# Optimization experiments

Measured on AMD Instinct MI355X. Metric: run time of the kernel, lower is better.

The kernel has to match this reference:

```python
import jax, jax.numpy as jnp
import numpy as np

D_HEAD = 64
EPS_NORM = 1e-6
EPS_COS = 1e-6


def rms_norm(x, scale, eps=EPS_NORM):
    mean_sq = jnp.mean(x * x, axis=-1, keepdims=True)
    return x * (scale * jax.lax.rsqrt(mean_sq + eps))


def setup_inputs() -> dict:
    key = jax.random.key(0)
    ks = jax.random.split(key, 8)
    b, l, d, d_ff = 2, 2048, 1024, 3072
    std = 1.0 / np.sqrt(d)
    return {
        "x": jax.random.normal(ks[0], (b, l, d), jnp.float32),
        "pos": jax.random.normal(ks[1], (b, l, 2), jnp.float32),
        "norm_scale": jnp.ones((d,), jnp.float32),
        "w_qkv": jax.random.normal(ks[2], (3 * d, d), jnp.float32) * std,
        "attn_scale": jnp.full((d // D_HEAD,), 10.0, jnp.float32),
        "w_out": jax.random.normal(ks[3], (d, d), jnp.float32) * std,
        "ff_norm_scale": jnp.ones((d,), jnp.float32),
        "w_up": jax.random.normal(ks[4], (2 * d_ff, d), jnp.float32) * std,
        "w_down": jax.random.normal(ks[5], (d, d_ff), jnp.float32) * (1.0 / np.sqrt(d_ff)),
    }


def reference(x, pos, norm_scale, w_qkv, attn_scale, w_out, ff_norm_scale, w_up, w_down):
    n, l, d = x.shape
    nh = d // D_HEAD

    # ---- self-attention block ----
    skip = x
    xn = rms_norm(x, norm_scale)
    qkv = xn @ w_qkv.T                                    # [n, l, 3d]
    qkv = qkv.reshape(n, l, 3, nh, D_HEAD).transpose(2, 0, 3, 1, 4)  # [3, n, nh, l, e]
    q, k, v = qkv[0], qkv[1], qkv[2]

    # cosine-similarity rescaling with per-head learned scale
    s = attn_scale[:, None, None]                         # [nh, 1, 1]
    sqrt_s = jnp.sqrt(s)
    q = q * (sqrt_s * jax.lax.rsqrt(jnp.sum(q * q, axis=-1, keepdims=True) + EPS_COS))
    k = k * (sqrt_s * jax.lax.rsqrt(jnp.sum(k * k, axis=-1, keepdims=True) + EPS_COS))

    # SDPA with scale=1.0 (no RoPE: rope_cls=None)
    scores = jnp.einsum("nhqe,nhke->nhqk", q, k)
    attn = jax.nn.softmax(scores, axis=-1)
    o = jnp.einsum("nhqk,nhke->nhqe", attn, v)            # [n, nh, l, e]
    o = o.transpose(0, 2, 1, 3).reshape(n, l, d)
    x = o @ w_out.T + skip

    # ---- feed-forward block (SwiGLU) ----
    skip = x
    xn = rms_norm(x, ff_norm_scale)
    u = xn @ w_up.T                                       # [n, l, 2*d_ff]
    a, g = jnp.split(u, 2, axis=-1)
    h = a * jax.nn.silu(g)
    x = h @ w_down.T + skip
    return x
```

## Files before the change

kernel.cpp:

```cpp
#include <hip/hip_runtime.h>
#include <cstdint>
#include <cstddef>
#include <cstdio>


typedef unsigned short u16;
typedef __bf16 bf16x8 __attribute__((ext_vector_type(8)));
typedef short  s16x4  __attribute__((ext_vector_type(4)));
typedef short  s16x8  __attribute__((ext_vector_type(8)));
typedef float  f32x4  __attribute__((ext_vector_type(4)));

__device__ __forceinline__ u16 f2b(float f) {
  return __builtin_bit_cast(u16, (__bf16)f);
}
__device__ __forceinline__ float b2f(u16 u) {
  return (float)__builtin_bit_cast(__bf16, u);
}

__device__ __forceinline__ void cp16(const u16* g, u16* l) {
  __builtin_amdgcn_global_load_lds(
      (__attribute__((address_space(1))) void*)(uintptr_t)g,
      (__attribute__((address_space(3))) void*)(uintptr_t)l,
      16, 0, 0);
}

template <int MODE, int BN>
__global__ __launch_bounds__(256) void gemm_bt(
    const u16* __restrict__ A, const u16* __restrict__ B,
    float* __restrict__ Cf, u16* __restrict__ Cb, const float* __restrict__ res,
    int M, int N, int K, int lda)
{
  constexpr int NI = BN / 32;
  __shared__ __align__(16) u16 lsA[128 * 64];
  __shared__ __align__(16) u16 lsB[BN * 64];
  const int t = threadIdx.x;
  const int w = t >> 6, lane = t & 63;
  const int wm = (w >> 1) * 64, wn = (w & 1) * (BN / 2);
  const int lr = lane & 15, quad = lane >> 4;
  const int cswz = lr & 7;
  const size_t rowA0 = (size_t)blockIdx.x * 128;
  const size_t rowB0 = (size_t)blockIdx.y * BN;
  const int kpb = K / (int)gridDim.z;
  const int kz0 = (int)blockIdx.z * kpb;

  f32x4 acc[4][NI] = {};

  for (int k0 = kz0; k0 < kz0 + kpb; k0 += 64) {
#pragma unroll
    for (int i = 0; i < 4; ++i) {
      const int id = i * 256 + t;
      const int r = id >> 3;
      const int c = ((id & 7) ^ (r & 7)) * 8;
      cp16(A + (rowA0 + r) * lda + k0 + c, lsA + id * 8);
    }
#pragma unroll
    for (int i = 0; i < BN / 32; ++i) {
      const int id = i * 256 + t;
      const int r = id >> 3;
      const int c = ((id & 7) ^ (r & 7)) * 8;
      cp16(B + (rowB0 + r) * (size_t)K + k0 + c, lsB + id * 8);
    }
    __syncthreads();
#pragma unroll
    for (int ks = 0; ks < 2; ++ks) {
      const int co = ((ks * 4 + quad) ^ cswz) * 8;
      bf16x8 af[4], bfr[NI];
#pragma unroll
      for (int i = 0; i < 4; ++i)
        af[i] = *(const bf16x8*)(lsA + (wm + i * 16 + lr) * 64 + co);
#pragma unroll
      for (int i = 0; i < NI; ++i)
        bfr[i] = *(const bf16x8*)(lsB + (wn + i * 16 + lr) * 64 + co);
#pragma unroll
      for (int mi = 0; mi < 4; ++mi)
#pragma unroll
        for (int ni = 0; ni < NI; ++ni)
          acc[mi][ni] = __builtin_amdgcn_mfma_f32_16x16x32_bf16(
              af[mi], bfr[ni], acc[mi][ni], 0, 0, 0);
    }
    __syncthreads();
  }

#pragma unroll
  for (int mi = 0; mi < 4; ++mi) {
#pragma unroll
    for (int r = 0; r < 4; ++r) {
      const size_t m = rowA0 + wm + mi * 16 + quad * 4 + r;
#pragma unroll
      for (int ni = 0; ni < NI; ++ni) {
        const size_t n = rowB0 + wn + ni * 16 + lr;
        const size_t o = m * (size_t)N + n;
        const float v = acc[mi][ni][r];
        if (MODE == 0) Cf[o] = v;
        else if (MODE == 1) Cf[o] = v + res[o];
        else if (MODE == 2) Cb[o] = f2b(v);
        else atomicAdd(&Cf[o], v);
      }
    }
  }
}

__global__ __launch_bounds__(256) void rmsnorm_k(
    const float* __restrict__ x, const float* __restrict__ g, u16* __restrict__ out)
{
  const int row = blockIdx.x;
  const int t = threadIdx.x;
  const float4 a = ((const float4*)(x + (size_t)row * 1024))[t];
  float ss = a.x * a.x + a.y * a.y + a.z * a.z + a.w * a.w;
#pragma unroll
  for (int o = 32; o; o >>= 1) ss += __shfl_xor(ss, o, 64);
  __shared__ float red[4];
  if ((t & 63) == 0) red[t >> 6] = ss;
  __syncthreads();
  ss = red[0] + red[1] + red[2] + red[3];
  const float r = rsqrtf(ss * (1.0f / 1024.0f) + 1e-6f);
  const float4 gg = ((const float4*)g)[t];
  ushort4 o4;
  o4.x = f2b(a.x * gg.x * r);
  o4.y = f2b(a.y * gg.y * r);
  o4.z = f2b(a.z * gg.z * r);
  o4.w = f2b(a.w * gg.w * r);
  ((ushort4*)out)[(size_t)row * 256 + t] = o4;
}

__global__ __launch_bounds__(256) void cvt_bf16_k(
    const float* __restrict__ in, u16* __restrict__ out)
{
  const size_t i = (size_t)blockIdx.x * 256 + threadIdx.x;
  const float4 v = ((const float4*)in)[i];
  ushort4 o4;
  o4.x = f2b(v.x); o4.y = f2b(v.y); o4.z = f2b(v.z); o4.w = f2b(v.w);
  ((ushort4*)out)[i] = o4;
}

__global__ __launch_bounds__(256) void qkv_prep_k(
    const u16* __restrict__ qkv, const float* __restrict__ attn_scale,
    u16* __restrict__ Qb, u16* __restrict__ Kb, u16* __restrict__ Vt)
{
  const int l0 = blockIdx.x * 64;
  const int h  = blockIdx.y;
  const int nb = blockIdx.z;
  const int t = threadIdx.x, w = t >> 6, lane = t & 63;
  __shared__ float lsV[64][65];
  const float sq = sqrtf(attn_scale[h]);
  const int head = nb * 16 + h;
#pragma unroll 4
  for (int i = 0; i < 16; ++i) {
    const int lrow = i * 4 + w;
    const int l = l0 + lrow;
    const u16* base = qkv + ((size_t)nb * 2048 + l) * 3072 + h * 64 + lane;
    const float qv = b2f(base[0]);
    const float kv = b2f(base[1024]);
    const float vv = b2f(base[2048]);
    float ssq = qv * qv, ssk = kv * kv;
#pragma unroll
    for (int o = 32; o; o >>= 1) {
      ssq += __shfl_xor(ssq, o, 64);
      ssk += __shfl_xor(ssk, o, 64);
    }
    const size_t gb = ((size_t)head * 2048 + l) * 64 + lane;
    Qb[gb] = f2b(qv * sq * rsqrtf(ssq + 1e-6f));
    Kb[gb] = f2b(kv * sq * rsqrtf(ssk + 1e-6f));
    lsV[lrow][lane] = vv;
  }
  __syncthreads();
  const int e = t >> 2, p = t & 3;
  union { u16 s[16]; uint4 v[2]; } tmp;
#pragma unroll
  for (int cc = 0; cc < 2; ++cc) {
    const int c = 2 * p + cc;
    const int kb = 32 * (c >> 2) + 4 * (c & 3);
#pragma unroll
    for (int i = 0; i < 4; ++i) {
      tmp.s[cc * 8 + i]     = f2b(lsV[kb + i][e]);
      tmp.s[cc * 8 + 4 + i] = f2b(lsV[kb + 16 + i][e]);
    }
  }
  u16* dst = Vt + ((size_t)head * 64 + e) * 2048 + l0 + p * 16;
  *(uint4*)dst = tmp.v[0];
  *(uint4*)(dst + 8) = tmp.v[1];
}

__global__ __launch_bounds__(256) void attn_k(
    const u16* __restrict__ Qb, const u16* __restrict__ Kb,
    const u16* __restrict__ Vt, u16* __restrict__ O)
{
  const int l0 = blockIdx.x * 64;
  const int head = blockIdx.y;
  const int nb = head >> 4, h = head & 15;
  const int t = threadIdx.x, w = t >> 6, lane = t & 63;
  const int lr = lane & 15, quad = lane >> 4;
  const int kh = w & 1, qh = w >> 1;
  __shared__ __align__(16) u16 lsKV[2][2][64 * 64];
  const size_t hb = (size_t)head << 17;

  const int sr = t >> 3;
  const int sc = ((t & 7) ^ (sr & 7)) * 8;
  const u16* Kg = Kb + hb + (size_t)sr * 64 + sc;
  const u16* Vg = Vt + hb + (size_t)sr * 2048 + sc;

  bf16x8 qf[2][2];
#pragma unroll
  for (int qb = 0; qb < 2; ++qb) {
    const u16* qp = Qb + hb + (size_t)(l0 + qh * 32 + qb * 16 + lr) * 64 + quad * 8;
    qf[qb][0] = *(const bf16x8*)qp;
    qf[qb][1] = *(const bf16x8*)(qp + 32);
  }

  f32x4 ot[2][4] = {};
  float rs[2] = {0.f, 0.f};

  cp16(Kg, lsKV[0][0] + t * 8);
  cp16(Kg + 32 * 64, lsKV[0][0] + 32 * 64 + t * 8);
  cp16(Vg, lsKV[0][1] + t * 8);
  cp16(Vg + 32 * 2048, lsKV[0][1] + 32 * 64 + t * 8);

  int cur = 0;
  for (int k0 = 0; k0 < 2048; k0 += 64) {
    __syncthreads();
    if (k0 + 64 < 2048) {
      const int nxt = cur ^ 1;
      const u16* Kn = Kg + (size_t)(k0 + 64) * 64;
      const u16* Vn = Vg + (k0 + 64);
      cp16(Kn, lsKV[nxt][0] + t * 8);
      cp16(Kn + 32 * 64, lsKV[nxt][0] + 32 * 64 + t * 8);
      cp16(Vn, lsKV[nxt][1] + t * 8);
      cp16(Vn + 32 * 2048, lsKV[nxt][1] + 32 * 64 + t * 8);
    }
    const u16* kb = lsKV[cur][0];
    const u16* vb = lsKV[cur][1];

    s16x4 pf[2][2];
#pragma unroll
    for (int ktl = 0; ktl < 2; ++ktl) {
      const int kt = kh * 2 + ktl;
      const int krow = (kt * 16 + lr) * 64;
      const int kswz = lr & 7;
      const bf16x8 a0 = *(const bf16x8*)(kb + krow + ((quad ^ kswz) << 3));
      const bf16x8 a1 = *(const bf16x8*)(kb + krow + (((4 + quad) ^ kswz) << 3));
#pragma unroll
      for (int qb = 0; qb < 2; ++qb) {
        f32x4 s = {};
        s = __builtin_amdgcn_mfma_f32_16x16x32_bf16(a0, qf[qb][0], s, 0, 0, 0);
        s = __builtin_amdgcn_mfma_f32_16x16x32_bf16(a1, qf[qb][1], s, 0, 0, 0);
#pragma unroll
        for (int r = 0; r < 4; ++r) {
          const float p = __expf(s[r]);
          rs[qb] += p;
          pf[qb][ktl][r] = (short)f2b(p);
        }
      }
    }
#pragma unroll
    for (int ei = 0; ei < 4; ++ei) {
      const int vrow = ei * 16 + lr;
      const s16x8 vv = *(const s16x8*)(vb + vrow * 64 + (((kh * 4 + quad) ^ (vrow & 7)) << 3));
      const s16x4 v0 = __builtin_shufflevector(vv, vv, 0, 1, 2, 3);
      const s16x4 v1 = __builtin_shufflevector(vv, vv, 4, 5, 6, 7);
#pragma unroll
      for (int qb = 0; qb < 2; ++qb) {
        ot[qb][ei] = __builtin_amdgcn_mfma_f32_16x16x16bf16_1k(v0, pf[qb][0], ot[qb][ei], 0, 0, 0);
        ot[qb][ei] = __builtin_amdgcn_mfma_f32_16x16x16bf16_1k(v1, pf[qb][1], ot[qb][ei], 0, 0, 0);
      }
    }
    cur ^= 1;
  }

#pragma unroll
  for (int qb = 0; qb < 2; ++qb) {
    rs[qb] += __shfl_xor(rs[qb], 16, 64);
    rs[qb] += __shfl_xor(rs[qb], 32, 64);
  }

  __syncthreads();
  float* mb = (float*)lsKV;
  if (kh == 1) {
    float* dst = mb + (qh * 64 + lane) * 34;
#pragma unroll
    for (int qb = 0; qb < 2; ++qb)
#pragma unroll
      for (int ei = 0; ei < 4; ++ei)
#pragma unroll
        for (int r = 0; r < 4; ++r)
          dst[qb * 16 + ei * 4 + r] = ot[qb][ei][r];
    dst[32] = rs[0];
    dst[33] = rs[1];
  }
  __syncthreads();
  if (kh == 0) {
    const float* src = mb + (qh * 64 + lane) * 34;
#pragma unroll
    for (int qb = 0; qb < 2; ++qb) {
      const float inv = 1.0f / (rs[qb] + src[32 + qb]);
      u16* ob = O + ((size_t)nb * 2048 + l0 + qh * 32 + qb * 16 + lr) * 1024 + h * 64 + quad * 4;
#pragma unroll
      for (int ei = 0; ei < 4; ++ei) {
        ushort4 o4;
        o4.x = f2b((ot[qb][ei][0] + src[qb * 16 + ei * 4 + 0]) * inv);
        o4.y = f2b((ot[qb][ei][1] + src[qb * 16 + ei * 4 + 1]) * inv);
        o4.z = f2b((ot[qb][ei][2] + src[qb * 16 + ei * 4 + 2]) * inv);
        o4.w = f2b((ot[qb][ei][3] + src[qb * 16 + ei * 4 + 3]) * inv);
        *(ushort4*)(ob + ei * 16) = o4;
      }
    }
  }
}

__global__ __launch_bounds__(256) void swiglu_k(u16* __restrict__ u)
{
  const unsigned j = ((unsigned)blockIdx.x * 256 + threadIdx.x) * 8;
  const unsigned row = j / 3072u, col = j % 3072u;
  u16* ap = u + (size_t)row * 6144 + col;
  union { u16 s[8]; uint4 v; } a, g, hh;
  a.v = *(const uint4*)ap;
  g.v = *(const uint4*)(ap + 3072);
#pragma unroll
  for (int i = 0; i < 8; ++i) {
    const float av = b2f(a.s[i]);
    const float gv = b2f(g.s[i]);
    hh.s[i] = f2b(av * (gv / (1.0f + __expf(-gv))));
  }
  *(uint4*)ap = hh.v;
}

static constexpr size_t WQKV_B = 0;
static constexpr size_t WOUT_B = WQKV_B + 6291456;
static constexpr size_t WUP_B  = WOUT_B + 2097152;
static constexpr size_t WDN_B  = WUP_B + 12582912;
static constexpr size_t XN_B   = WDN_B + 6291456;
static constexpr size_t Q_B    = XN_B + 8388608;
static constexpr size_t K_B    = Q_B + 8388608;
static constexpr size_t VT_B   = K_B + 8388608;
static constexpr size_t O_B    = VT_B + 8388608;
static constexpr size_t BIG_B  = O_B + 8388608;
static constexpr size_t WS_NEED = BIG_B + 50331648;

extern "C" void kernel_launch(void* const* d_in, const int* in_sizes, int n_in,
                              void* d_out, int out_size, void* d_ws, size_t ws_size,
                              hipStream_t stream)
{
  (void)in_sizes; (void)n_in; (void)out_size;
  if (ws_size < WS_NEED) {
    fprintf(stderr, "kernel_launch: ws_size %zu < required %zu\n", ws_size, WS_NEED);
    return;
  }
  const float* x          = (const float*)d_in[0];
  const float* norm_scale = (const float*)d_in[2];
  const float* w_qkv      = (const float*)d_in[3];
  const float* attn_scale = (const float*)d_in[4];
  const float* w_out      = (const float*)d_in[5];
  const float* ff_scale   = (const float*)d_in[6];
  const float* w_up       = (const float*)d_in[7];
  const float* w_down     = (const float*)d_in[8];
  float* out = (float*)d_out;
  char* ws = (char*)d_ws;

  u16* wqkv_b = (u16*)(ws + WQKV_B);
  u16* wout_b = (u16*)(ws + WOUT_B);
  u16* wup_b  = (u16*)(ws + WUP_B);
  u16* wdn_b  = (u16*)(ws + WDN_B);
  u16* xn     = (u16*)(ws + XN_B);
  u16* Qb     = (u16*)(ws + Q_B);
  u16* Kb     = (u16*)(ws + K_B);
  u16* Vtb    = (u16*)(ws + VT_B);
  u16* Ob     = (u16*)(ws + O_B);
  u16* qkvb   = (u16*)(ws + BIG_B);
  u16* ub     = (u16*)(ws + BIG_B);

  cvt_bf16_k<<<3072, 256, 0, stream>>>(w_qkv, wqkv_b);
  cvt_bf16_k<<<1024, 256, 0, stream>>>(w_out, wout_b);
  cvt_bf16_k<<<6144, 256, 0, stream>>>(w_up,  wup_b);
  cvt_bf16_k<<<3072, 256, 0, stream>>>(w_down, wdn_b);

  rmsnorm_k<<<4096, 256, 0, stream>>>(x, norm_scale, xn);
  gemm_bt<2, 128><<<dim3(32, 24), 256, 0, stream>>>(xn, wqkv_b, nullptr, qkvb,
                                                    nullptr, 4096, 3072, 1024, 1024);
  qkv_prep_k<<<dim3(32, 16, 2), 256, 0, stream>>>(qkvb, attn_scale, Qb, Kb, Vtb);
  attn_k<<<dim3(32, 32), 256, 0, stream>>>(Qb, Kb, Vtb, Ob);
  gemm_bt<1, 64><<<dim3(32, 16), 256, 0, stream>>>(Ob, wout_b, out, nullptr, x,
                                                   4096, 1024, 1024, 1024);
  rmsnorm_k<<<4096, 256, 0, stream>>>(out, ff_scale, xn);
  gemm_bt<2, 128><<<dim3(32, 48), 256, 0, stream>>>(xn, wup_b, nullptr, ub, nullptr,
                                                    4096, 6144, 1024, 1024);
  swiglu_k<<<6144, 256, 0, stream>>>(ub);
  gemm_bt<3, 128><<<dim3(32, 8, 2), 256, 0, stream>>>(ub, wdn_b, out, nullptr,
                                                      nullptr, 4096, 1024, 3072, 6144);
}
```

Measured before the change: 378.7 us.

## Fuse SwiGLU into up-projection GEMM, drop split-K atomics, merge weight casts

The up-projection GEMM now loads matching value and gate weight rows into one tile and applies SwiGLU in the epilogue, writing a compact 3072-wide bf16 hidden buffer. This removes the separate swiglu pass and the 6144-wide intermediate round trip. The down-projection changes from split-K with atomic adds to a single-pass GEMM (BN=64) that adds the residual in the epilogue, and the four weight-conversion launches are merged into one. The single-pass down GEMM has 512 blocks with a longer K loop, so it trades the atomics away for possibly lower parallelism.

```diff
diff --git a/kernel.cpp b/kernel.cpp
--- a/kernel.cpp
+++ b/kernel.cpp
@@ -40,12 +40,10 @@
   const int cswz = lr & 7;
   const size_t rowA0 = (size_t)blockIdx.x * 128;
   const size_t rowB0 = (size_t)blockIdx.y * BN;
-  const int kpb = K / (int)gridDim.z;
-  const int kz0 = (int)blockIdx.z * kpb;
 
   f32x4 acc[4][NI] = {};
 
-  for (int k0 = kz0; k0 < kz0 + kpb; k0 += 64) {
+  for (int k0 = 0; k0 < K; k0 += 64) {
 #pragma unroll
     for (int i = 0; i < 4; ++i) {
       const int id = i * 256 + t;
@@ -93,8 +91,78 @@
         const float v = acc[mi][ni][r];
         if (MODE == 0) Cf[o] = v;
         else if (MODE == 1) Cf[o] = v + res[o];
-        else if (MODE == 2) Cb[o] = f2b(v);
-        else atomicAdd(&Cf[o], v);
+        else Cb[o] = f2b(v);
+      }
+    }
+  }
+}
+
+__global__ __launch_bounds__(256) void gemm_up_swiglu_k(
+    const u16* __restrict__ A, const u16* __restrict__ B, u16* __restrict__ H)
+{
+  __shared__ __align__(16) u16 lsA[128 * 64];
+  __shared__ __align__(16) u16 lsB[128 * 64];
+  const int t = threadIdx.x;
+  const int w = t >> 6, lane = t & 63;
+  const int wm = (w >> 1) * 64, wn = (w & 1) * 32;
+  const int lr = lane & 15, quad = lane >> 4;
+  const int cswz = lr & 7;
+  const size_t rowA0 = (size_t)blockIdx.x * 128;
+  const int j0 = blockIdx.y * 64;
+
+  f32x4 aa[4][2] = {}, ag[4][2] = {};
+
+  for (int k0 = 0; k0 < 1024; k0 += 64) {
+#pragma unroll
+    for (int i = 0; i < 4; ++i) {
+      const int id = i * 256 + t;
+      const int r = id >> 3;
+      const int c = ((id & 7) ^ (r & 7)) * 8;
+      cp16(A + (rowA0 + r) * 1024 + k0 + c, lsA + id * 8);
+    }
+#pragma unroll
+    for (int i = 0; i < 4; ++i) {
+      const int id = i * 256 + t;
+      const int r = id >> 3;
+      const int c = ((id & 7) ^ (r & 7)) * 8;
+      const int gr = (r < 64) ? (j0 + r) : (3072 + j0 + (r - 64));
+      cp16(B + (size_t)gr * 1024 + k0 + c, lsB + id * 8);
+    }
+    __syncthreads();
+#pragma unroll
+    for (int ks = 0; ks < 2; ++ks) {
+      const int co = ((ks * 4 + quad) ^ cswz) * 8;
+      bf16x8 af[4], ba[2], bg[2];
+#pragma unroll
+      for (int i = 0; i < 4; ++i)
+        af[i] = *(const bf16x8*)(lsA + (wm + i * 16 + lr) * 64 + co);
+#pragma unroll
+      for (int i = 0; i < 2; ++i) {
+        ba[i] = *(const bf16x8*)(lsB + (wn + i * 16 + lr) * 64 + co);
+        bg[i] = *(const bf16x8*)(lsB + (64 + wn + i * 16 + lr) * 64 + co);
+      }
+#pragma unroll
+      for (int mi = 0; mi < 4; ++mi)
+#pragma unroll
+        for (int ni = 0; ni < 2; ++ni) {
+          aa[mi][ni] = __builtin_amdgcn_mfma_f32_16x16x32_bf16(af[mi], ba[ni], aa[mi][ni], 0, 0, 0);
+          ag[mi][ni] = __builtin_amdgcn_mfma_f32_16x16x32_bf16(af[mi], bg[ni], ag[mi][ni], 0, 0, 0);
+        }
+    }
+    __syncthreads();
+  }
+
+#pragma unroll
+  for (int mi = 0; mi < 4; ++mi) {
+#pragma unroll
+    for (int r = 0; r < 4; ++r) {
+      const size_t m = rowA0 + wm + mi * 16 + quad * 4 + r;
+#pragma unroll
+      for (int ni = 0; ni < 2; ++ni) {
+        const int j = j0 + wn + ni * 16 + lr;
+        const float a = aa[mi][ni][r];
+        const float g = ag[mi][ni][r];
+        H[m * 3072 + j] = f2b(a * (g / (1.0f + __expf(-g))));
       }
     }
   }
@@ -123,14 +191,23 @@
   ((ushort4*)out)[(size_t)row * 256 + t] = o4;
 }
 
-__global__ __launch_bounds__(256) void cvt_bf16_k(
-    const float* __restrict__ in, u16* __restrict__ out)
-{
-  const size_t i = (size_t)blockIdx.x * 256 + threadIdx.x;
-  const float4 v = ((const float4*)in)[i];
+__global__ __launch_bounds__(256) void cvt_all_k(
+    const float* __restrict__ s0, const float* __restrict__ s1,
+    const float* __restrict__ s2, const float* __restrict__ s3,
+    u16* __restrict__ d0, u16* __restrict__ d1,
+    u16* __restrict__ d2, u16* __restrict__ d3)
+{
+  const int b = blockIdx.x;
+  const float* s; u16* d; int off;
+  if (b < 3072)       { s = s0; d = d0; off = b; }
+  else if (b < 4096)  { s = s1; d = d1; off = b - 3072; }
+  else if (b < 10240) { s = s2; d = d2; off = b - 4096; }
+  else                { s = s3; d = d3; off = b - 10240; }
+  const size_t i = (size_t)off * 256 + threadIdx.x;
+  const float4 v = ((const float4*)s)[i];
   ushort4 o4;
   o4.x = f2b(v.x); o4.y = f2b(v.y); o4.z = f2b(v.z); o4.w = f2b(v.w);
-  ((ushort4*)out)[i] = o4;
+  ((ushort4*)d)[i] = o4;
 }
 
 __global__ __launch_bounds__(256) void qkv_prep_k(
@@ -306,23 +383,6 @@
   }
 }
 
-__global__ __launch_bounds__(256) void swiglu_k(u16* __restrict__ u)
-{
-  const unsigned j = ((unsigned)blockIdx.x * 256 + threadIdx.x) * 8;
-  const unsigned row = j / 3072u, col = j % 3072u;
-  u16* ap = u + (size_t)row * 6144 + col;
-  union { u16 s[8]; uint4 v; } a, g, hh;
-  a.v = *(const uint4*)ap;
-  g.v = *(const uint4*)(ap + 3072);
-#pragma unroll
-  for (int i = 0; i < 8; ++i) {
-    const float av = b2f(a.s[i]);
-    const float gv = b2f(g.s[i]);
-    hh.s[i] = f2b(av * (gv / (1.0f + __expf(-gv))));
-  }
-  *(uint4*)ap = hh.v;
-}
-
 static constexpr size_t WQKV_B = 0;
 static constexpr size_t WOUT_B = WQKV_B + 6291456;
 static constexpr size_t WUP_B  = WOUT_B + 2097152;
@@ -365,12 +425,10 @@
   u16* Vtb    = (u16*)(ws + VT_B);
   u16* Ob     = (u16*)(ws + O_B);
   u16* qkvb   = (u16*)(ws + BIG_B);
-  u16* ub     = (u16*)(ws + BIG_B);
-
-  cvt_bf16_k<<<3072, 256, 0, stream>>>(w_qkv, wqkv_b);
-  cvt_bf16_k<<<1024, 256, 0, stream>>>(w_out, wout_b);
-  cvt_bf16_k<<<6144, 256, 0, stream>>>(w_up,  wup_b);
-  cvt_bf16_k<<<3072, 256, 0, stream>>>(w_down, wdn_b);
+  u16* hb     = (u16*)(ws + BIG_B);
+
+  cvt_all_k<<<13312, 256, 0, stream>>>(w_qkv, w_out, w_up, w_down,
+                                       wqkv_b, wout_b, wup_b, wdn_b);
 
   rmsnorm_k<<<4096, 256, 0, stream>>>(x, norm_scale, xn);
   gemm_bt<2, 128><<<dim3(32, 24), 256, 0, stream>>>(xn, wqkv_b, nullptr, qkvb,
@@ -380,9 +438,7 @@
   gemm_bt<1, 64><<<dim3(32, 16), 256, 0, stream>>>(Ob, wout_b, out, nullptr, x,
                                                    4096, 1024, 1024, 1024);
   rmsnorm_k<<<4096, 256, 0, stream>>>(out, ff_scale, xn);
-  gemm_bt<2, 128><<<dim3(32, 48), 256, 0, stream>>>(xn, wup_b, nullptr, ub, nullptr,
-                                                    4096, 6144, 1024, 1024);
-  swiglu_k<<<6144, 256, 0, stream>>>(ub);
-  gemm_bt<3, 128><<<dim3(32, 8, 2), 256, 0, stream>>>(ub, wdn_b, out, nullptr,
-                                                      nullptr, 4096, 1024, 3072, 6144);
-}
+  gemm_up_swiglu_k<<<dim3(32, 48), 256, 0, stream>>>(xn, wup_b, hb);
+  gemm_bt<1, 64><<<dim3(32, 16), 256, 0, stream>>>(hb, wdn_b, out, nullptr, out,
+                                                   4096, 1024, 3072, 3072);
+}
```

Result: faster. 351.5 us (-7.2%).
